# Kernel optimization log

Hardware: AMD Instinct MI355X
Metric: run time of the kernel (lower is better)

Reference implementation:

```python
import jax, jax.numpy as jnp
import numpy as np

B, L, N, P = 64, 512, 321, 720   # batch, seq_len, enc_in, pred_len
E, R, CID, H = 8, 32, 32, 64     # experts, rank, channel_identity_dim, router hidden


def setup_inputs() -> dict:
    key = jax.random.key(0)
    ks = jax.random.split(key, 9)
    return {
        "x": jax.random.normal(ks[0], (B, L, N), dtype=jnp.float32),
        # per-channel identity embedding for the router
        "ident": jax.random.normal(ks[1], (N, CID), dtype=jnp.float32) * 0.02,
        # router MLP: CID -> H -> E
        "rw1": jax.random.normal(ks[2], (CID, H), dtype=jnp.float32) * (1.0 / np.sqrt(CID)),
        "rb1": jnp.zeros((H,), dtype=jnp.float32),
        "rw2": jax.random.normal(ks[3], (H, E), dtype=jnp.float32) * (1.0 / np.sqrt(H)),
        "rb2": jnp.zeros((E,), dtype=jnp.float32),
        # low-rank experts: L -> R -> P
        "w1": jax.random.normal(ks[4], (E, L, R), dtype=jnp.float32) * (1.0 / np.sqrt(L)),
        "w2": jax.random.normal(ks[5], (E, R, P), dtype=jnp.float32) * (1.0 / np.sqrt(R)),
        "b": jnp.zeros((E, P), dtype=jnp.float32),
    }


def reference(x, ident, rw1, rb1, rw2, rb2, w1, w2, b):
    # RevIN-style normalization over the time dim (torch std is unbiased, ddof=1)
    mean = jnp.mean(x, axis=1, keepdims=True)                    # [B,1,N]
    std = jnp.std(x, axis=1, keepdims=True, ddof=1) + 1e-6       # [B,1,N]
    xn = ((x - mean) / std).transpose(0, 2, 1)                   # [B,N,L]

    # per-channel MoE router (soft routing over experts)
    hidden = jax.nn.relu(ident @ rw1 + rb1)                      # [N,H]
    gate = jax.nn.softmax(hidden @ rw2 + rb2, axis=-1)           # [N,E]

    # low-rank expert projections L -> R -> P
    h = jnp.einsum('bnl,elr->bner', xn, w1)                      # [B,N,E,R]
    y = jnp.einsum('bner,erp->bnep', h, w2) + b                  # [B,N,E,P]
    y = jnp.einsum('bnep,ne->bnp', y, gate)                      # [B,N,P]

    pred = y.transpose(0, 2, 1)                                  # [B,P,N]
    return pred * std + mean
```

## Files before the change

### kernel.cpp

```cpp
#include <hip/hip_runtime.h>
#include <math.h>

#define B_ 64
#define L_ 512
#define N_ 321
#define P_ 720
#define E_ 8
#define R_ 32
#define CID_ 32
#define H_ 64
#define ER_ 256
#define KB2 288
#define HGROWS 384

typedef __attribute__((ext_vector_type(8))) short bf16x8;
typedef __attribute__((ext_vector_type(4))) float f32x4;
typedef __attribute__((ext_vector_type(8))) unsigned short u16x8;
typedef __attribute__((ext_vector_type(4))) unsigned short u16x4;

#define OFF_GATE 0
#define OFF_MEAN 2568
#define OFF_SDEV 27144
#define OFF_W1K  51720
#define OFF_W2X  117256
#define OFF_HG   220936

__device__ __forceinline__ unsigned short f2bf(float f) {
    unsigned u = __float_as_uint(f);
    u += 0x7fffu + ((u >> 16) & 1u);
    return (unsigned short)(u >> 16);
}
__device__ __forceinline__ float bf2f(unsigned short h) {
    return __uint_as_float(((unsigned)h) << 16);
}

__global__ void router_kernel(const float* __restrict__ ident,
                              const float* __restrict__ rw1, const float* __restrict__ rb1,
                              const float* __restrict__ rw2, const float* __restrict__ rb2,
                              float* __restrict__ gate) {
    int n = blockIdx.x;
    int t = threadIdx.x;
    __shared__ float hid[H_];
    __shared__ float lg[E_];
    float acc = rb1[t];
    #pragma unroll
    for (int c = 0; c < CID_; ++c)
        acc = fmaf(ident[n*CID_ + c], rw1[c*H_ + t], acc);
    hid[t] = fmaxf(acc, 0.f);
    __syncthreads();
    if (t < E_) {
        float a = rb2[t];
        #pragma unroll
        for (int h = 0; h < H_; ++h) a = fmaf(hid[h], rw2[h*E_ + t], a);
        lg[t] = a;
    }
    __syncthreads();
    if (t == 0) {
        float m = lg[0];
        #pragma unroll
        for (int e = 1; e < E_; ++e) m = fmaxf(m, lg[e]);
        float s = 0.f, ex[E_];
        #pragma unroll
        for (int e = 0; e < E_; ++e) { ex[e] = expf(lg[e] - m); s += ex[e]; }
        float inv = 1.f / s;
        #pragma unroll
        for (int e = 0; e < E_; ++e) gate[n*E_ + e] = ex[e] * inv;
    }
}

__global__ void prep_kernel(const float* __restrict__ w1, const float* __restrict__ w2,
                            const float* __restrict__ bias,
                            unsigned short* __restrict__ w1k, unsigned short* __restrict__ w2x) {
    int bid = blockIdx.x, t = threadIdx.x;
    if (bid < 128) {
        #pragma unroll
        for (int r = 0; r < 2; ++r) {
            int g = bid*1024 + r*512 + t;
            int er = g >> 9, l = g & 511;
            w1k[g] = f2bf(w1[(size_t)(er >> 5)*(L_*R_) + (size_t)l*R_ + (er & 31)]);
        }
    } else {
        int p = bid - 128;
        if (t < KB2) {
            unsigned short v;
            if (t < ER_)            v = f2bf(w2[(size_t)t*P_ + p]);
            else if (t < ER_ + E_)  v = f2bf(bias[(size_t)(t - ER_)*P_ + p]);
            else if (t == ER_ + E_) v = 0x3f80;
            else                    v = 0;
            w2x[(size_t)p*KB2 + t] = v;
        }
    }
}

__global__ __launch_bounds__(512) void stats_kernel(
        const float* __restrict__ x, float* __restrict__ meanv, float* __restrict__ sdev) {
    __shared__ float red1[8][64], red2[8][64];
    const int bid = blockIdx.x;
    const int b   = bid / 6;
    const int n0  = (bid % 6) * 64;
    const int t   = threadIdx.x;
    const int xn  = t & 63;
    const int q   = t >> 6;
    const int gn  = n0 + xn;
    const int gnc = (gn < N_) ? gn : (N_ - 1);
    const float* xp = x + (size_t)b*L_*N_ + gnc;

    float s1 = 0.f, s2 = 0.f;
    #pragma unroll 8
    for (int i = 0; i < 64; ++i) {
        float v = xp[(size_t)(q*64 + i)*N_];
        s1 += v; s2 = fmaf(v, v, s2);
    }
    red1[q][xn] = s1; red2[q][xn] = s2;
    __syncthreads();
    if (t < 64) {
        float a = 0.f, qq = 0.f;
        #pragma unroll
        for (int kk = 0; kk < 8; ++kk) { a += red1[kk][t]; qq += red2[kk][t]; }
        float mean = a * (1.f/L_);
        float var = (qq - (float)L_*mean*mean) * (1.f/(L_-1));
        var = fmaxf(var, 0.f);
        size_t id = (size_t)b*HGROWS + n0 + t;
        meanv[id] = mean;
        sdev[id]  = sqrtf(var) + 1e-6f;
    }
}

__global__ __launch_bounds__(512, 4) void gemm1_kernel(
        const float* __restrict__ x, const unsigned short* __restrict__ w1k,
        const float* __restrict__ gate, const float* __restrict__ meanv,
        const float* __restrict__ sdev, unsigned short* __restrict__ hg) {
    __shared__ unsigned short buf[2][64][128];

    const int bid = blockIdx.x;
    const int xcd = bid & 7;
    const int idx = bid >> 3;
    const int b   = (xcd << 3) + idx / 6;
    const int n0  = (idx % 6) * 64;

    const int tid  = threadIdx.x;
    const int lane = tid & 63;
    const int wave = tid >> 6;
    const int l15  = lane & 15;
    const int kgrp = lane >> 4;

    const int xn  = lane;
    const int gn  = n0 + xn;
    const int gnc = (gn < N_) ? gn : (N_ - 1);
    const float* xp = x + (size_t)b*L_*N_ + gnc;
    const float mean_n = meanv[(size_t)b*HGROWS + n0 + ((gn < N_) ? xn : 0)];
    const int swz = (xn & 7) << 4;
    char* myrow0 = (char*)&buf[0][xn][0];
    char* myrow1 = (char*)&buf[1][xn][0];

    const unsigned short* apA = w1k + (size_t)(wave*32 + l15)*L_;
    const unsigned short* apB = w1k + (size_t)(wave*32 + 16 + l15)*L_;
    const int rsw = (l15 & 7) << 4;

    float v[16];
    f32x4 acc[2][4];
    #pragma unroll
    for (int i = 0; i < 2; ++i)
        #pragma unroll
        for (int j = 0; j < 4; ++j) acc[i][j] = (f32x4){0.f,0.f,0.f,0.f};

#define LOADV(rd_) {                                                            \
    const int kb = (rd_)*128 + wave*16;                                         \
    _Pragma("unroll")                                                           \
    for (int i_ = 0; i_ < 16; ++i_)                                             \
        v[i_] = xp[(size_t)(kb + i_)*N_]; }
#define STOREV(rd_) {                                                           \
    char* dst = ((rd_) & 1) ? myrow1 : myrow0;                                  \
    u16x8 pk0, pk1;                                                             \
    _Pragma("unroll")                                                           \
    for (int i_ = 0; i_ < 8; ++i_)  pk0[i_] = f2bf(v[i_] - mean_n);             \
    _Pragma("unroll")                                                           \
    for (int i_ = 0; i_ < 8; ++i_)  pk1[i_] = f2bf(v[8+i_] - mean_n);           \
    *(u16x8*)(dst + ((wave*32)      ^ swz)) = pk0;                              \
    *(u16x8*)(dst + ((wave*32 + 16) ^ swz)) = pk1; }

    LOADV(0);
    STOREV(0);
    __syncthreads();

    bf16x8 af[4][2];
#define LDA(s_, kk_) { af[s_][0] = *(const bf16x8*)&apA[(kk_)*32 + kgrp*8];      \
                       af[s_][1] = *(const bf16x8*)&apB[(kk_)*32 + kgrp*8]; }
    LDA(0, 0); LDA(1, 1);

    #pragma unroll
    for (int rd = 0; rd < 4; ++rd) {
        if (rd < 3) LOADV(rd + 1);
        const unsigned short (*cb)[128] = buf[rd & 1];
        #pragma unroll
        for (int ks = 0; ks < 4; ++ks) {
            const int kk = rd*4 + ks;
            if (kk + 2 < 16) LDA((kk + 2) & 3, kk + 2);
            const int cbyte = ks*64 + kgrp*16;
            bf16x8 bfr[4];
            #pragma unroll
            for (int fn = 0; fn < 4; ++fn)
                bfr[fn] = *(const bf16x8*)((const char*)&cb[fn*16 + l15][0] + (cbyte ^ rsw));
            #pragma unroll
            for (int fn = 0; fn < 4; ++fn) {
                acc[0][fn] = __builtin_amdgcn_mfma_f32_16x16x32_bf16(af[kk & 3][0], bfr[fn], acc[0][fn], 0, 0, 0);
                acc[1][fn] = __builtin_amdgcn_mfma_f32_16x16x32_bf16(af[kk & 3][1], bfr[fn], acc[1][fn], 0, 0, 0);
            }
        }
        if (rd < 3) STOREV(rd + 1);
        __syncthreads();
    }
#undef LDA
#undef LOADV
#undef STOREV

    unsigned short* hgb = hg + ((size_t)b * HGROWS + n0) * KB2;
    const float* mrow = meanv + (size_t)b*HGROWS + n0;
    const float* srow = sdev  + (size_t)b*HGROWS + n0;
    #pragma unroll
    for (int fm = 0; fm < 2; ++fm) {
        int er0 = wave*32 + fm*16 + kgrp*4;
        int e = er0 >> 5;
        #pragma unroll
        for (int fn = 0; fn < 4; ++fn) {
            int nl = fn*16 + l15;
            int gnn = n0 + nl; if (gnn > N_-1) gnn = N_-1;
            float g = gate[gnn*E_ + e];
            u16x4 pk;
            #pragma unroll
            for (int j = 0; j < 4; ++j)
                pk[j] = f2bf(g * acc[fm][fn][j]);
            *(u16x4*)&hgb[(size_t)nl*KB2 + er0] = pk;
        }
    }
    {
        int nl = tid >> 3, seg = tid & 7;
        int gnn = n0 + nl; if (gnn > N_-1) gnn = N_-1;
        float sd = srow[nl], m = mrow[nl];
        u16x4 pk;
        #pragma unroll
        for (int jj = 0; jj < 4; ++jj) {
            int k = seg*4 + jj;
            float vv = (k < E_) ? gate[gnn*E_ + k] * sd : ((k == E_) ? m : 0.f);
            pk[jj] = f2bf(vv);
        }
        *(u16x4*)&hgb[(size_t)nl*KB2 + ER_ + seg*4] = pk;
    }
}

#define HGS 296
__global__ __launch_bounds__(512, 6) void gemm2_kernel(
        const unsigned short* __restrict__ hg, const unsigned short* __restrict__ w2x,
        float* __restrict__ out) {
    __shared__ __align__(16) char smem[64 * HGS * 2];
    unsigned short* hgL = (unsigned short*)smem;
    const int bid = blockIdx.x;
    const int xcd = bid & 7;
    const int idx = bid >> 3;
    const int b   = (xcd << 3) + idx / 36;
    const int rem = idx % 36;
    const int p0  = (rem / 6) * 128;
    const int n0  = (rem % 6) * 64;

    const int tid  = threadIdx.x;
    const int lane = tid & 63;
    const int wave = tid >> 6;
    const int l15  = lane & 15;
    const int kgrp = lane >> 4;

    const unsigned short* hgb = hg + ((size_t)b * HGROWS + n0) * KB2;
    #pragma unroll
    for (int it = 0; it < 5; ++it) {
        int c = tid + it*512;
        if (c < 64*36) {
            int row = c / 36, col = c % 36;
            *(u16x8*)&hgL[(size_t)row*HGS + col*8] =
                *(const u16x8*)&hgb[(size_t)row*KB2 + col*8];
        }
    }
    __syncthreads();

    int prow = p0 + wave*16 + l15; if (prow > P_-1) prow = P_-1;
    const unsigned short* ap = w2x + (size_t)prow*KB2;
    f32x4 o[4];
    #pragma unroll
    for (int j = 0; j < 4; ++j) o[j] = (f32x4){0.f,0.f,0.f,0.f};
    #pragma unroll
    for (int ks = 0; ks < 9; ++ks) {
        bf16x8 afr = *(const bf16x8*)&ap[ks*32 + kgrp*8];
        #pragma unroll
        for (int fn = 0; fn < 4; ++fn) {
            bf16x8 bfr = *(const bf16x8*)&hgL[(size_t)(fn*16 + l15)*HGS + ks*32 + kgrp*8];
            o[fn] = __builtin_amdgcn_mfma_f32_16x16x32_bf16(afr, bfr, o[fn], 0, 0, 0);
        }
    }
    __syncthreads();

    float* patch = (float*)smem + wave * 1088;
    #pragma unroll
    for (int fn = 0; fn < 4; ++fn)
        #pragma unroll
        for (int j = 0; j < 4; ++j)
            patch[(kgrp*4 + j)*68 + fn*16 + l15] = o[fn][j];
    const int pw0 = p0 + wave*16;
    #pragma unroll
    for (int pass = 0; pass < 4; ++pass) {
        int ploc = pass*4 + kgrp;
        f32x4 v = *(const f32x4*)&patch[ploc*68 + l15*4];
        int p = pw0 + ploc;
        int n = n0 + l15*4;
        if (p < P_) {
            float* orow = out + ((size_t)b*P_ + p)*N_;
            if (n + 3 < N_) {
                *(f32x4*)&orow[n] = v;
            } else {
                #pragma unroll
                for (int j = 0; j < 4; ++j)
                    if (n + j < N_) orow[n + j] = v[j];
            }
        }
    }
}

extern "C" void kernel_launch(void* const* d_in, const int* in_sizes, int n_in,
                              void* d_out, int out_size, void* d_ws, size_t ws_size,
                              hipStream_t stream) {
    const float* x     = (const float*)d_in[0];
    const float* ident = (const float*)d_in[1];
    const float* rw1   = (const float*)d_in[2];
    const float* rb1   = (const float*)d_in[3];
    const float* rw2   = (const float*)d_in[4];
    const float* rb2   = (const float*)d_in[5];
    const float* w1    = (const float*)d_in[6];
    const float* w2    = (const float*)d_in[7];
    const float* bias  = (const float*)d_in[8];
    float* out = (float*)d_out;
    float* ws  = (float*)d_ws;

    float* gate  = ws + OFF_GATE;
    float* meanv = ws + OFF_MEAN;
    float* sdev  = ws + OFF_SDEV;
    unsigned short* w1k = (unsigned short*)(ws + OFF_W1K);
    unsigned short* w2x = (unsigned short*)(ws + OFF_W2X);
    unsigned short* hg  = (unsigned short*)(ws + OFF_HG);

    router_kernel<<<N_, 64, 0, stream>>>(ident, rw1, rb1, rw2, rb2, gate);
    prep_kernel<<<128 + 720, 512, 0, stream>>>(w1, w2, bias, w1k, w2x);
    stats_kernel<<<384, 512, 0, stream>>>(x, meanv, sdev);
    gemm1_kernel<<<dim3(384), 512, 0, stream>>>(x, w1k, gate, meanv, sdev, hg);
    gemm2_kernel<<<dim3(2304), 512, 0, stream>>>(hg, w2x, out);
}
```

Before: 74.23 us.

## Fuse per-channel stats into gemm1 and fold mean subtraction via w1 column sums

Removes the separate stats kernel that reads all of x once more. gemm1 now accumulates sum and sum-of-squares while staging raw x, and corrects the GEMM result afterwards with mean times the precomputed bf16-rounded column sums of w1 (computed in extra prep blocks). This saves a full pass over x and one launch. In exchange, gemm1 uses more shared memory and registers, and feeding raw rather than centred x to bf16 may lose precision when the mean is large.

```diff
diff --git a/kernel.cpp b/kernel.cpp
--- a/kernel.cpp
+++ b/kernel.cpp
@@ -19,11 +19,10 @@
 typedef __attribute__((ext_vector_type(4))) unsigned short u16x4;
 
 #define OFF_GATE 0
-#define OFF_MEAN 2568
-#define OFF_SDEV 27144
-#define OFF_W1K  51720
-#define OFF_W2X  117256
-#define OFF_HG   220936
+#define OFF_CS1  2568
+#define OFF_W1K  2824
+#define OFF_W2X  68360
+#define OFF_HG   172040
 
 __device__ __forceinline__ unsigned short f2bf(float f) {
     unsigned u = __float_as_uint(f);
@@ -70,7 +69,9 @@
 
 __global__ void prep_kernel(const float* __restrict__ w1, const float* __restrict__ w2,
                             const float* __restrict__ bias,
-                            unsigned short* __restrict__ w1k, unsigned short* __restrict__ w2x) {
+                            unsigned short* __restrict__ w1k, unsigned short* __restrict__ w2x,
+                            float* __restrict__ cs1) {
+    __shared__ float red[16][32];
     int bid = blockIdx.x, t = threadIdx.x;
     if (bid < 128) {
         #pragma unroll
@@ -79,7 +80,7 @@
             int er = g >> 9, l = g & 511;
             w1k[g] = f2bf(w1[(size_t)(er >> 5)*(L_*R_) + (size_t)l*R_ + (er & 31)]);
         }
-    } else {
+    } else if (bid < 848) {
         int p = bid - 128;
         if (t < KB2) {
             unsigned short v;
@@ -89,48 +90,29 @@
             else                    v = 0;
             w2x[(size_t)p*KB2 + t] = v;
         }
-    }
-}
-
-__global__ __launch_bounds__(512) void stats_kernel(
-        const float* __restrict__ x, float* __restrict__ meanv, float* __restrict__ sdev) {
-    __shared__ float red1[8][64], red2[8][64];
-    const int bid = blockIdx.x;
-    const int b   = bid / 6;
-    const int n0  = (bid % 6) * 64;
-    const int t   = threadIdx.x;
-    const int xn  = t & 63;
-    const int q   = t >> 6;
-    const int gn  = n0 + xn;
-    const int gnc = (gn < N_) ? gn : (N_ - 1);
-    const float* xp = x + (size_t)b*L_*N_ + gnc;
-
-    float s1 = 0.f, s2 = 0.f;
-    #pragma unroll 8
-    for (int i = 0; i < 64; ++i) {
-        float v = xp[(size_t)(q*64 + i)*N_];
-        s1 += v; s2 = fmaf(v, v, s2);
-    }
-    red1[q][xn] = s1; red2[q][xn] = s2;
-    __syncthreads();
-    if (t < 64) {
-        float a = 0.f, qq = 0.f;
-        #pragma unroll
-        for (int kk = 0; kk < 8; ++kk) { a += red1[kk][t]; qq += red2[kk][t]; }
-        float mean = a * (1.f/L_);
-        float var = (qq - (float)L_*mean*mean) * (1.f/(L_-1));
-        var = fmaxf(var, 0.f);
-        size_t id = (size_t)b*HGROWS + n0 + t;
-        meanv[id] = mean;
-        sdev[id]  = sqrtf(var) + 1e-6f;
+    } else {
+        int e = bid - 848;
+        int q = t >> 5, r = t & 31;
+        float s = 0.f;
+        for (int l = q; l < L_; l += 16)
+            s += bf2f(f2bf(w1[(size_t)e*(L_*R_) + (size_t)l*R_ + r]));
+        red[q][r] = s;
+        __syncthreads();
+        if (q == 0) {
+            #pragma unroll
+            for (int qq = 1; qq < 16; ++qq) s += red[qq][r];
+            cs1[e*32 + r] = s;
+        }
     }
 }
 
 __global__ __launch_bounds__(512, 4) void gemm1_kernel(
         const float* __restrict__ x, const unsigned short* __restrict__ w1k,
-        const float* __restrict__ gate, const float* __restrict__ meanv,
-        const float* __restrict__ sdev, unsigned short* __restrict__ hg) {
+        const float* __restrict__ gate, const float* __restrict__ cs1,
+        unsigned short* __restrict__ hg) {
     __shared__ unsigned short buf[2][64][128];
+    __shared__ float red1[8][64], red2[8][64];
+    __shared__ float meanS[64], sdS[64];
 
     const int bid = blockIdx.x;
     const int xcd = bid & 7;
@@ -148,7 +130,6 @@
     const int gn  = n0 + xn;
     const int gnc = (gn < N_) ? gn : (N_ - 1);
     const float* xp = x + (size_t)b*L_*N_ + gnc;
-    const float mean_n = meanv[(size_t)b*HGROWS + n0 + ((gn < N_) ? xn : 0)];
     const int swz = (xn & 7) << 4;
     char* myrow0 = (char*)&buf[0][xn][0];
     char* myrow1 = (char*)&buf[1][xn][0];
@@ -157,6 +138,7 @@
     const unsigned short* apB = w1k + (size_t)(wave*32 + 16 + l15)*L_;
     const int rsw = (l15 & 7) << 4;
 
+    float s1 = 0.f, s2 = 0.f;
     float v[16];
     f32x4 acc[2][4];
     #pragma unroll
@@ -173,9 +155,12 @@
     char* dst = ((rd_) & 1) ? myrow1 : myrow0;                                  \
     u16x8 pk0, pk1;                                                             \
     _Pragma("unroll")                                                           \
-    for (int i_ = 0; i_ < 8; ++i_)  pk0[i_] = f2bf(v[i_] - mean_n);             \
+    for (int i_ = 0; i_ < 8; ++i_) {                                            \
+        s1 += v[i_]; s2 = fmaf(v[i_], v[i_], s2); pk0[i_] = f2bf(v[i_]); }      \
     _Pragma("unroll")                                                           \
-    for (int i_ = 0; i_ < 8; ++i_)  pk1[i_] = f2bf(v[8+i_] - mean_n);           \
+    for (int i_ = 0; i_ < 8; ++i_) {                                            \
+        float f_ = v[8+i_];                                                     \
+        s1 += f_; s2 = fmaf(f_, f_, s2); pk1[i_] = f2bf(f_); }                  \
     *(u16x8*)(dst + ((wave*32)      ^ swz)) = pk0;                              \
     *(u16x8*)(dst + ((wave*32 + 16) ^ swz)) = pk1; }
 
@@ -214,29 +199,44 @@
 #undef LOADV
 #undef STOREV
 
+    red1[wave][xn] = s1;
+    red2[wave][xn] = s2;
+    __syncthreads();
+    if (tid < 64) {
+        float a = 0.f, qq = 0.f;
+        #pragma unroll
+        for (int kk = 0; kk < 8; ++kk) { a += red1[kk][tid]; qq += red2[kk][tid]; }
+        float mean = a * (1.f/L_);
+        float var = (qq - (float)L_*mean*mean) * (1.f/(L_-1));
+        var = fmaxf(var, 0.f);
+        meanS[tid] = mean;
+        sdS[tid]   = sqrtf(var) + 1e-6f;
+    }
+    __syncthreads();
+
     unsigned short* hgb = hg + ((size_t)b * HGROWS + n0) * KB2;
-    const float* mrow = meanv + (size_t)b*HGROWS + n0;
-    const float* srow = sdev  + (size_t)b*HGROWS + n0;
     #pragma unroll
     for (int fm = 0; fm < 2; ++fm) {
         int er0 = wave*32 + fm*16 + kgrp*4;
         int e = er0 >> 5;
+        f32x4 c4 = *(const f32x4*)&cs1[er0];
         #pragma unroll
         for (int fn = 0; fn < 4; ++fn) {
             int nl = fn*16 + l15;
             int gnn = n0 + nl; if (gnn > N_-1) gnn = N_-1;
             float g = gate[gnn*E_ + e];
+            float m = meanS[nl];
             u16x4 pk;
             #pragma unroll
             for (int j = 0; j < 4; ++j)
-                pk[j] = f2bf(g * acc[fm][fn][j]);
+                pk[j] = f2bf(g * (acc[fm][fn][j] - m * c4[j]));
             *(u16x4*)&hgb[(size_t)nl*KB2 + er0] = pk;
         }
     }
     {
         int nl = tid >> 3, seg = tid & 7;
         int gnn = n0 + nl; if (gnn > N_-1) gnn = N_-1;
-        float sd = srow[nl], m = mrow[nl];
+        float sd = sdS[nl], m = meanS[nl];
         u16x4 pk;
         #pragma unroll
         for (int jj = 0; jj < 4; ++jj) {
@@ -337,16 +337,14 @@
     float* out = (float*)d_out;
     float* ws  = (float*)d_ws;
 
-    float* gate  = ws + OFF_GATE;
-    float* meanv = ws + OFF_MEAN;
-    float* sdev  = ws + OFF_SDEV;
+    float* gate = ws + OFF_GATE;
+    float* cs1  = ws + OFF_CS1;
     unsigned short* w1k = (unsigned short*)(ws + OFF_W1K);
     unsigned short* w2x = (unsigned short*)(ws + OFF_W2X);
     unsigned short* hg  = (unsigned short*)(ws + OFF_HG);
 
     router_kernel<<<N_, 64, 0, stream>>>(ident, rw1, rb1, rw2, rb2, gate);
-    prep_kernel<<<128 + 720, 512, 0, stream>>>(w1, w2, bias, w1k, w2x);
-    stats_kernel<<<384, 512, 0, stream>>>(x, meanv, sdev);
-    gemm1_kernel<<<dim3(384), 512, 0, stream>>>(x, w1k, gate, meanv, sdev, hg);
+    prep_kernel<<<856, 512, 0, stream>>>(w1, w2, bias, w1k, w2x, cs1);
+    gemm1_kernel<<<dim3(384), 512, 0, stream>>>(x, w1k, gate, cs1, hg);
     gemm2_kernel<<<dim3(2304), 512, 0, stream>>>(hg, w2x, out);
 }
```

Result: faster. 66.61 us (-10.3%).
